# Optimization experiments

Measured on AMD Instinct MI355X. Metric: run time of the kernel, lower is better.

Reference implementation:

```python
import jax, jax.numpy as jnp
import numpy as np

H = 768
NH = 12
HD = H // NH  # 64
WINDOW = 64  # module's self.window_size; band keeps |i-j| <= WINDOW//2


def setup_inputs() -> dict:
    key = jax.random.key(0)
    ks = jax.random.split(key, 9)
    s = 0.02
    return {
        "hidden_states": jax.random.normal(ks[0], (4, 2048, H), dtype=jnp.float32),
        "Wq": jax.random.normal(ks[1], (H, H), dtype=jnp.float32) * s,
        "bq": jnp.zeros((H,), dtype=jnp.float32),
        "Wk": jax.random.normal(ks[2], (H, H), dtype=jnp.float32) * s,
        "bk": jnp.zeros((H,), dtype=jnp.float32),
        "Wv": jax.random.normal(ks[3], (H, H), dtype=jnp.float32) * s,
        "bv": jnp.zeros((H,), dtype=jnp.float32),
        "Wo": jax.random.normal(ks[4], (H, H), dtype=jnp.float32) * s,
        "bo": jnp.zeros((H,), dtype=jnp.float32),
    }


def _attn(hidden_states, Wq, bq, Wk, bk, Wv, bv, Wo, bo):
    B, S, _ = hidden_states.shape
    # projections (torch Linear uses y = x @ W.T + b; here W is stored already transposed)
    q = (hidden_states @ Wq + bq).reshape(B, S, NH, HD).transpose(0, 2, 1, 3)
    k = (hidden_states @ Wk + bk).reshape(B, S, NH, HD).transpose(0, 2, 1, 3)
    v = (hidden_states @ Wv + bv).reshape(B, S, NH, HD).transpose(0, 2, 1, 3)
    # dense scores [B, NH, S, S], faithful to the original O(S^2) computation
    scores = jnp.einsum("bhqd,bhkd->bhqk", q, k) / jnp.sqrt(jnp.float32(HD))
    # sliding-window band mask: keep j in [i - W//2, i + W//2]
    i = jnp.arange(S)[:, None]
    j = jnp.arange(S)[None, :]
    band = jnp.abs(i - j) <= (WINDOW // 2)
    scores = jnp.where(band[None, None, :, :], scores, jnp.float32(-1e9))
    probs = jax.nn.softmax(scores, axis=-1)
    ctx = jnp.einsum("bhqk,bhkd->bhqd", probs, v)
    ctx = ctx.transpose(0, 2, 1, 3).reshape(B, S, H)
    return ctx @ Wo + bo


def reference(hidden_states, Wq, bq, Wk, bk, Wv, bv, Wo, bo):
    return _attn(hidden_states, Wq, bq, Wk, bk, Wv, bv, Wo, bo)
```

## Files before the change

kernel.cpp:

```cpp
#include <hip/hip_runtime.h>
#include <hip/hip_bf16.h>

#define NHEAD 12
#define HD 64
#define SEQ 2048
#define NB 4
#define HDIM 768
#define MTOT (NB * SEQ)

typedef float f32x4 __attribute__((ext_vector_type(4)));
typedef float f32x16 __attribute__((ext_vector_type(16)));
typedef short s16x8 __attribute__((ext_vector_type(8)));
typedef unsigned short u16x8 __attribute__((ext_vector_type(8)));

__device__ inline unsigned short f2bf(float f) {
    union { float f; unsigned u; } v; v.f = f;
    unsigned r = v.u + 0x7fffu + ((v.u >> 16) & 1u);
    return (unsigned short)(r >> 16);
}
__device__ inline float bf2f(unsigned short u) {
    union { unsigned u; float f; } v; v.u = ((unsigned)u) << 16;
    return v.f;
}
__device__ inline unsigned pack_bf2(float a, float b) {
    return (unsigned)f2bf(a) | ((unsigned)f2bf(b) << 16);
}
__device__ inline s16x8 mk_frag(uint2 lo, uint2 hi) {
    union { unsigned u[4]; s16x8 v; } r;
    r.u[0] = lo.x; r.u[1] = lo.y; r.u[2] = hi.x; r.u[3] = hi.y;
    return r.v;
}
__device__ inline void gload_lds16(const unsigned short* g, void* lds_base) {
    __builtin_amdgcn_global_load_lds(
        (const __attribute__((address_space(1))) void*)g,
        (__attribute__((address_space(3))) void*)lds_base, 16, 0, 0);
}

#define MFMA(acc, a, b) \
    acc = __builtin_amdgcn_mfma_f32_16x16x32_bf16((a), (b), (acc), 0, 0, 0)
#define MFMA32(acc, a, b) \
    acc = __builtin_amdgcn_mfma_f32_32x32x16_bf16((a), (b), (acc), 0, 0, 0)

__global__ __launch_bounds__(256) void prep_kernel(
    const float* __restrict__ X,
    const float* __restrict__ Wq, const float* __restrict__ Wk,
    const float* __restrict__ Wv, const float* __restrict__ Wo,
    unsigned short* __restrict__ Xb,
    unsigned short* __restrict__ Wt, unsigned short* __restrict__ Wot)
{
    __shared__ __align__(16) unsigned short ts[64][68];
    const int t = threadIdx.x;
    const int bid = blockIdx.x;

    if (bid < 3072) {
        const int i = (bid * 256 + t) * 8;
        float4 a = *(const float4*)(X + i);
        float4 b = *(const float4*)(X + i + 4);
        ushort4 wa, wb;
        wa.x = f2bf(a.x); wa.y = f2bf(a.y); wa.z = f2bf(a.z); wa.w = f2bf(a.w);
        wb.x = f2bf(b.x); wb.y = f2bf(b.y); wb.z = f2bf(b.z); wb.w = f2bf(b.w);
        *(ushort4*)(Xb + i) = wa;
        *(ushort4*)(Xb + i + 4) = wb;
        return;
    }

    const int id = bid - 3072;
    const int z  = id / 144;
    const int rem = id - z * 144;
    const int k0 = (rem / 12) * 64, n0 = (rem % 12) * 64;
    const float* W = (z == 0) ? Wq : (z == 1) ? Wk : (z == 2) ? Wv : Wo;
    unsigned short* D = (z < 3) ? (Wt + (size_t)z * HDIM * HDIM) : Wot;

    const int kr = (t >> 4) * 4;
    const int nc = (t & 15) * 4;
    #pragma unroll
    for (int r = 0; r < 4; r++) {
        float4 v = *(const float4*)(W + (size_t)(k0 + kr + r) * HDIM + n0 + nc);
        ushort4 w;
        w.x = f2bf(v.x); w.y = f2bf(v.y); w.z = f2bf(v.z); w.w = f2bf(v.w);
        *(ushort4*)&ts[kr + r][nc] = w;
    }
    __syncthreads();
    const int nr = t >> 2;
    const int kc = (t & 3) * 16;
    #pragma unroll
    for (int j4 = 0; j4 < 4; j4++) {
        ushort4 w;
        w.x = ts[kc + j4 * 4 + 0][nr];
        w.y = ts[kc + j4 * 4 + 1][nr];
        w.z = ts[kc + j4 * 4 + 2][nr];
        w.w = ts[kc + j4 * 4 + 3][nr];
        *(ushort4*)(D + (size_t)(n0 + nr) * HDIM + k0 + kc + j4 * 4) = w;
    }
}

template<int MODE, int BM>
__global__ __launch_bounds__(256) void gemm_kernel(
    const unsigned short* __restrict__ A,
    const unsigned short* __restrict__ Bt,
    const float* __restrict__ bias0, const float* __restrict__ bias1,
    const float* __restrict__ bias2,
    unsigned short* __restrict__ Qb, unsigned short* __restrict__ Kb,
    unsigned short* __restrict__ Vb, float* __restrict__ out)
{
    constexpr int MF  = BM / 64;
    constexpr int CHA = BM / 32;

    __shared__ __align__(16) unsigned short As[BM * 64];
    __shared__ __align__(16) unsigned short Bs[128 * 64];

    const int t = threadIdx.x;
    const int lane = t & 63;
    const int wid = t >> 6;
    const int wm = wid >> 1, wn = wid & 1;
    const int l31 = lane & 31;
    const int lh = lane >> 5;

    const int m0 = blockIdx.x * BM;
    const int n0 = blockIdx.y * 128;

    int srow[4], scol[4];
    #pragma unroll
    for (int i = 0; i < 4; i++) {
        const int p = i * 4096 + t * 16;
        const int row = p >> 7;
        const int cb = p & 127;
        srow[i] = row;
        scol[i] = (cb ^ ((row & 7) << 4)) >> 1;
    }

    f32x16 acc[MF][2] = {};

    for (int k0 = 0; k0 < HDIM; k0 += 64) {
        __syncthreads();
        #pragma unroll
        for (int i = 0; i < CHA; i++)
            gload_lds16(A + (size_t)(m0 + srow[i]) * HDIM + k0 + scol[i],
                        (char*)As + i * 4096 + wid * 1024);
        #pragma unroll
        for (int i = 0; i < 4; i++)
            gload_lds16(Bt + (size_t)(n0 + srow[i]) * HDIM + k0 + scol[i],
                        (char*)Bs + i * 4096 + wid * 1024);
        __syncthreads();

        const int sw = (l31 & 7) << 4;
        #pragma unroll
        for (int kv = 0; kv < 4; kv++) {
            const int cb = (kv * 32 + lh * 16) ^ sw;
            s16x8 av[MF];
            #pragma unroll
            for (int j = 0; j < MF; j++)
                av[j] = *(const s16x8*)((const char*)As +
                        (wm * (BM / 2) + j * 32 + l31) * 128 + cb);
            s16x8 b0 = *(const s16x8*)((const char*)Bs + (wn * 64 +      l31) * 128 + cb);
            s16x8 b1 = *(const s16x8*)((const char*)Bs + (wn * 64 + 32 + l31) * 128 + cb);
            #pragma unroll
            for (int j = 0; j < MF; j++) {
                MFMA32(acc[j][0], av[j], b0);
                MFMA32(acc[j][1], av[j], b1);
            }
        }
    }

    if (MODE == 0) {
        const int z = n0 / HDIM;
        const float* bias = (z == 0) ? bias0 : (z == 1) ? bias1 : bias2;
        const float scale = (z == 0) ? 0.125f : 1.0f;
        unsigned short* dst = (z == 0) ? Qb : (z == 1) ? Kb : Vb;
        #pragma unroll
        for (int fm = 0; fm < MF; fm++) {
            #pragma unroll
            for (int fn = 0; fn < 2; fn++) {
                const int coll = (n0 - z * HDIM) + wn * 64 + fn * 32 + l31;
                const float bc = bias[coll];
                const int h = coll >> 6, d = coll & 63;
                #pragma unroll
                for (int reg = 0; reg < 16; reg++) {
                    const int rowD = (reg & 3) + 8 * (reg >> 2) + 4 * lh;
                    const int m = m0 + wm * (BM / 2) + fm * 32 + rowD;
                    const int b = m >> 11, s = m & (SEQ - 1);
                    const size_t idx = (z == 2)
                        ? ((((size_t)b * NHEAD + h) * HD + d) * SEQ + s)
                        : ((((size_t)b * NHEAD + h) * SEQ + s) * HD + d);
                    dst[idx] = f2bf((acc[fm][fn][reg] + bc) * scale);
                }
            }
        }
    } else {
        #pragma unroll
        for (int fm = 0; fm < MF; fm++) {
            #pragma unroll
            for (int fn = 0; fn < 2; fn++) {
                const int col = n0 + wn * 64 + fn * 32 + l31;
                const float bc = bias0[col];
                #pragma unroll
                for (int reg = 0; reg < 16; reg++) {
                    const int rowD = (reg & 3) + 8 * (reg >> 2) + 4 * lh;
                    const int m = m0 + wm * (BM / 2) + fm * 32 + rowD;
                    out[(size_t)m * HDIM + col] = acc[fm][fn][reg] + bc;
                }
            }
        }
    }
}

__global__ __launch_bounds__(512) void attn_mfma(
    const unsigned short* __restrict__ Qb, const unsigned short* __restrict__ Kb,
    const unsigned short* __restrict__ Vtg, unsigned short* __restrict__ Cb)
{
    __shared__ __align__(16) unsigned short Ks[192][72];
    __shared__ __align__(16) unsigned short Vs[64][208];

    const int t = threadIdx.x;
    const int lane = t & 63;
    const int wq = t >> 6;
    const int woff = wq * 16;
    const int g = lane >> 4, r16 = lane & 15;

    const int lid = blockIdx.y * 16 + blockIdx.x;
    const int wg = (lid & 7) * 96 + (lid >> 3);
    const int q0 = (wg & 15) * 128;
    const int bh = wg >> 4;

    const int b = bh / NHEAD, h = bh - b * NHEAD;
    const size_t base  = (size_t)bh * SEQ * HD;
    const size_t vbase = (size_t)bh * HD * SEQ;
    const int kstart = q0 - 32;
    const bool interior = (kstart >= 0) && (kstart + 191 < SEQ);

    #pragma unroll
    for (int i = 0; i < 3; i++) {
        const int u = i * 512 + t;
        const int row = u >> 3, c16 = (u & 7) * 8;
        const int s = kstart + row;
        if (s >= 0 && s < SEQ) {
            *(u16x8*)&Ks[row][c16] =
                *(const u16x8*)(Kb + base + (size_t)s * HD + c16);
        } else {
            const u16x8 z = {};
            *(u16x8*)&Ks[row][c16] = z;
        }
    }
    {
        const int row = t >> 3, c0 = (t & 7) * 24;
        const unsigned short* src = Vtg + vbase + (size_t)row * SEQ + kstart + c0;
        if (interior) {
            #pragma unroll
            for (int j = 0; j < 3; j++)
                *(u16x8*)&Vs[row][c0 + 8 * j] = *(const u16x8*)(src + 8 * j);
        } else {
            for (int e = 0; e < 24; e++) {
                const int s = kstart + c0 + e;
                Vs[row][c0 + e] = (s >= 0 && s < SEQ) ? src[e] : (unsigned short)0;
            }
        }
        if (t < 128) {
            const u16x8 z = {};
            *(u16x8*)&Vs[t >> 1][192 + (t & 1) * 8] = z;
        }
    }

    s16x8 qf[2];
    {
        const unsigned short* gq = Qb + base + (size_t)(q0 + woff + r16) * HD;
        #pragma unroll
        for (int c = 0; c < 2; c++)
            qf[c] = mk_frag(*(const uint2*)(gq + c * 32 + 4 * g),
                            *(const uint2*)(gq + c * 32 + 16 + 4 * g));
    }
    __syncthreads();

    f32x4 sacc[5] = {};
    #pragma unroll
    for (int mf = 0; mf < 5; mf++) {
        const unsigned short* p = &Ks[woff + mf * 16 + r16][0];
        #pragma unroll
        for (int c = 0; c < 2; c++) {
            s16x8 kf = mk_frag(*(const uint2*)(p + c * 32 + 4 * g),
                               *(const uint2*)(p + c * 32 + 16 + 4 * g));
            MFMA(sacc[mf], kf, qf[c]);
        }
    }

    float mx = -1e30f;
    #pragma unroll
    for (int mf = 0; mf < 5; mf++) {
        #pragma unroll
        for (int r = 0; r < 4; r++) {
            const int rel = mf * 16 + 4 * g + r - r16;
            const int sg = kstart + woff + mf * 16 + 4 * g + r;
            const bool ok = (rel >= 0) && (rel <= 64) && (sg >= 0) && (sg < SEQ);
            const float v = ok ? sacc[mf][r] : -1e30f;
            sacc[mf][r] = v;
            mx = fmaxf(mx, v);
        }
    }
    mx = fmaxf(mx, __shfl_xor(mx, 16));
    mx = fmaxf(mx, __shfl_xor(mx, 32));
    float l = 0.f;
    #pragma unroll
    for (int mf = 0; mf < 5; mf++) {
        #pragma unroll
        for (int r = 0; r < 4; r++) {
            const float e = __expf(sacc[mf][r] - mx);
            sacc[mf][r] = e;
            l += e;
        }
    }
    l += __shfl_xor(l, 16);
    l += __shfl_xor(l, 32);
    const float inv = 1.f / l;

    s16x8 pf[3];
    #pragma unroll
    for (int c = 0; c < 3; c++) {
        union { unsigned u[4]; s16x8 v; } pv;
        pv.u[0] = pack_bf2(sacc[2 * c][0] * inv, sacc[2 * c][1] * inv);
        pv.u[1] = pack_bf2(sacc[2 * c][2] * inv, sacc[2 * c][3] * inv);
        if (c < 2) {
            pv.u[2] = pack_bf2(sacc[2 * c + 1][0] * inv, sacc[2 * c + 1][1] * inv);
            pv.u[3] = pack_bf2(sacc[2 * c + 1][2] * inv, sacc[2 * c + 1][3] * inv);
        } else {
            pv.u[2] = 0; pv.u[3] = 0;
        }
        pf[c] = pv.v;
    }

    f32x4 cacc[4] = {};
    #pragma unroll
    for (int nf = 0; nf < 4; nf++) {
        const unsigned short* p = &Vs[nf * 16 + r16][woff];
        #pragma unroll
        for (int c = 0; c < 3; c++) {
            s16x8 vf = mk_frag(*(const uint2*)(p + c * 32 + 4 * g),
                               *(const uint2*)(p + c * 32 + 16 + 4 * g));
            MFMA(cacc[nf], pf[c], vf);
        }
    }

    #pragma unroll
    for (int nf = 0; nf < 4; nf++) {
        #pragma unroll
        for (int r = 0; r < 4; r++) {
            const int ql = woff + 4 * g + r;
            const int d = nf * 16 + r16;
            Cb[(((size_t)b * SEQ + q0 + ql) * NHEAD + h) * HD + d] = f2bf(cacc[nf][r]);
        }
    }
}

extern "C" void kernel_launch(void* const* d_in, const int* in_sizes, int n_in,
                              void* d_out, int out_size, void* d_ws, size_t ws_size,
                              hipStream_t stream)
{
    const float* X  = (const float*)d_in[0];
    const float* Wq = (const float*)d_in[1];
    const float* bq = (const float*)d_in[2];
    const float* Wk = (const float*)d_in[3];
    const float* bk = (const float*)d_in[4];
    const float* Wv = (const float*)d_in[5];
    const float* bv = (const float*)d_in[6];
    const float* Wo = (const float*)d_in[7];
    const float* bo = (const float*)d_in[8];
    float* out = (float*)d_out;

    char* ws = (char*)d_ws;
    unsigned short* Xb  = (unsigned short*)ws;
    unsigned short* Cb  = Xb;
    unsigned short* Vt  = (unsigned short*)(ws + 12582912);
    unsigned short* Wtp = (unsigned short*)(ws + 25165824);
    unsigned short* Wot = (unsigned short*)(ws + 28704768);
    unsigned short* Qb  = (unsigned short*)d_out;
    unsigned short* Kb  = (unsigned short*)((char*)d_out + 12582912);

    prep_kernel<<<dim3(3648), 256, 0, stream>>>(X, Wq, Wk, Wv, Wo, Xb, Wtp, Wot);
    gemm_kernel<0, 64><<<dim3(128, 18), 256, 0, stream>>>(Xb, Wtp, bq, bk, bv, Qb, Kb, Vt, nullptr);
    attn_mfma<<<dim3(16, 48), 512, 0, stream>>>(Qb, Kb, Vt, Cb);
    gemm_kernel<1, 64><<<dim3(128, 6), 256, 0, stream>>>(Cb, Wot, bo, nullptr, nullptr,
                                                         nullptr, nullptr, nullptr, out);
}
```

Measured before the change: 107.7 us.

## Fuse X fp32-to-bf16 conversion into QKV GEMM and coalesce attention output stores

Removes the separate X conversion pass from the prep kernel. The QKV GEMM now loads fp32 X directly, converts it to bf16 in registers and writes it into swizzled LDS, with the M tile raised to 128. The attention epilogue stages its context tile through LDS so global stores are 16-byte vectors instead of scattered 2-byte writes. This saves a full bf16 round trip of X through memory and improves store coalescing, at the cost of synchronous register-staged A loads instead of direct global-to-LDS, plus extra barriers in attention.

```diff
diff --git a/kernel.cpp b/kernel.cpp
--- a/kernel.cpp
+++ b/kernel.cpp
@@ -42,29 +42,13 @@
     acc = __builtin_amdgcn_mfma_f32_32x32x16_bf16((a), (b), (acc), 0, 0, 0)
 
 __global__ __launch_bounds__(256) void prep_kernel(
-    const float* __restrict__ X,
     const float* __restrict__ Wq, const float* __restrict__ Wk,
     const float* __restrict__ Wv, const float* __restrict__ Wo,
-    unsigned short* __restrict__ Xb,
     unsigned short* __restrict__ Wt, unsigned short* __restrict__ Wot)
 {
     __shared__ __align__(16) unsigned short ts[64][68];
     const int t = threadIdx.x;
-    const int bid = blockIdx.x;
-
-    if (bid < 3072) {
-        const int i = (bid * 256 + t) * 8;
-        float4 a = *(const float4*)(X + i);
-        float4 b = *(const float4*)(X + i + 4);
-        ushort4 wa, wb;
-        wa.x = f2bf(a.x); wa.y = f2bf(a.y); wa.z = f2bf(a.z); wa.w = f2bf(a.w);
-        wb.x = f2bf(b.x); wb.y = f2bf(b.y); wb.z = f2bf(b.z); wb.w = f2bf(b.w);
-        *(ushort4*)(Xb + i) = wa;
-        *(ushort4*)(Xb + i + 4) = wb;
-        return;
-    }
-
-    const int id = bid - 3072;
+    const int id = blockIdx.x;
     const int z  = id / 144;
     const int rem = id - z * 144;
     const int k0 = (rem / 12) * 64, n0 = (rem % 12) * 64;
@@ -96,6 +80,7 @@
 
 template<int MODE, int BM>
 __global__ __launch_bounds__(256) void gemm_kernel(
+    const float* __restrict__ Xf,
     const unsigned short* __restrict__ A,
     const unsigned short* __restrict__ Bt,
     const float* __restrict__ bias0, const float* __restrict__ bias1,
@@ -119,27 +104,49 @@
     const int m0 = blockIdx.x * BM;
     const int n0 = blockIdx.y * 128;
 
-    int srow[4], scol[4];
+    int srow[4], scb[4], sswb[4];
     #pragma unroll
     for (int i = 0; i < 4; i++) {
         const int p = i * 4096 + t * 16;
         const int row = p >> 7;
         const int cb = p & 127;
         srow[i] = row;
-        scol[i] = (cb ^ ((row & 7) << 4)) >> 1;
+        scb[i] = cb;
+        sswb[i] = cb ^ ((row & 7) << 4);
     }
 
     f32x16 acc[MF][2] = {};
 
     for (int k0 = 0; k0 < HDIM; k0 += 64) {
+        float4 fa[CHA][2];
+        if (MODE == 0) {
+            #pragma unroll
+            for (int i = 0; i < CHA; i++) {
+                const float* src = Xf + (size_t)(m0 + srow[i]) * HDIM + k0 + (scb[i] >> 1);
+                fa[i][0] = *(const float4*)src;
+                fa[i][1] = *(const float4*)(src + 4);
+            }
+        }
         __syncthreads();
-        #pragma unroll
-        for (int i = 0; i < CHA; i++)
-            gload_lds16(A + (size_t)(m0 + srow[i]) * HDIM + k0 + scol[i],
-                        (char*)As + i * 4096 + wid * 1024);
+        if (MODE == 0) {
+            #pragma unroll
+            for (int i = 0; i < CHA; i++) {
+                u16x8 w;
+                w[0] = f2bf(fa[i][0].x); w[1] = f2bf(fa[i][0].y);
+                w[2] = f2bf(fa[i][0].z); w[3] = f2bf(fa[i][0].w);
+                w[4] = f2bf(fa[i][1].x); w[5] = f2bf(fa[i][1].y);
+                w[6] = f2bf(fa[i][1].z); w[7] = f2bf(fa[i][1].w);
+                *(u16x8*)((char*)As + srow[i] * 128 + sswb[i]) = w;
+            }
+        } else {
+            #pragma unroll
+            for (int i = 0; i < CHA; i++)
+                gload_lds16(A + (size_t)(m0 + srow[i]) * HDIM + k0 + (sswb[i] >> 1),
+                            (char*)As + i * 4096 + wid * 1024);
+        }
         #pragma unroll
         for (int i = 0; i < 4; i++)
-            gload_lds16(Bt + (size_t)(n0 + srow[i]) * HDIM + k0 + scol[i],
+            gload_lds16(Bt + (size_t)(n0 + srow[i]) * HDIM + k0 + (sswb[i] >> 1),
                         (char*)Bs + i * 4096 + wid * 1024);
         __syncthreads();
 
@@ -338,14 +345,25 @@
         }
     }
 
+    __syncthreads();
+    unsigned short* Cs = &Ks[0][0];
     #pragma unroll
     for (int nf = 0; nf < 4; nf++) {
         #pragma unroll
         for (int r = 0; r < 4; r++) {
             const int ql = woff + 4 * g + r;
             const int d = nf * 16 + r16;
-            Cb[(((size_t)b * SEQ + q0 + ql) * NHEAD + h) * HD + d] = f2bf(cacc[nf][r]);
-        }
+            Cs[ql * 72 + d] = f2bf(cacc[nf][r]);
+        }
+    }
+    __syncthreads();
+
+    #pragma unroll
+    for (int i = 0; i < 2; i++) {
+        const int u = i * 512 + t;
+        const int row = u >> 3, c16 = (u & 7) * 8;
+        u16x8 w = *(const u16x8*)&Cs[row * 72 + c16];
+        *(u16x8*)(Cb + (((size_t)b * SEQ + q0 + row) * NHEAD + h) * HD + c16) = w;
     }
 }
 
@@ -365,17 +383,17 @@
     float* out = (float*)d_out;
 
     char* ws = (char*)d_ws;
-    unsigned short* Xb  = (unsigned short*)ws;
-    unsigned short* Cb  = Xb;
+    unsigned short* Cb  = (unsigned short*)ws;
     unsigned short* Vt  = (unsigned short*)(ws + 12582912);
     unsigned short* Wtp = (unsigned short*)(ws + 25165824);
     unsigned short* Wot = (unsigned short*)(ws + 28704768);
     unsigned short* Qb  = (unsigned short*)d_out;
     unsigned short* Kb  = (unsigned short*)((char*)d_out + 12582912);
 
-    prep_kernel<<<dim3(3648), 256, 0, stream>>>(X, Wq, Wk, Wv, Wo, Xb, Wtp, Wot);
-    gemm_kernel<0, 64><<<dim3(128, 18), 256, 0, stream>>>(Xb, Wtp, bq, bk, bv, Qb, Kb, Vt, nullptr);
+    prep_kernel<<<dim3(576), 256, 0, stream>>>(Wq, Wk, Wv, Wo, Wtp, Wot);
+    gemm_kernel<0, 128><<<dim3(64, 18), 256, 0, stream>>>(X, nullptr, Wtp, bq, bk, bv,
+                                                          Qb, Kb, Vt, nullptr);
     attn_mfma<<<dim3(16, 48), 512, 0, stream>>>(Qb, Kb, Vt, Cb);
-    gemm_kernel<1, 64><<<dim3(128, 6), 256, 0, stream>>>(Cb, Wot, bo, nullptr, nullptr,
-                                                         nullptr, nullptr, nullptr, out);
-}
+    gemm_kernel<1, 64><<<dim3(128, 6), 256, 0, stream>>>(nullptr, Cb, Wot, bo, nullptr,
+                                                         nullptr, nullptr, nullptr, nullptr, out);
+}
```

Result: slower. 114.9 us (+6.7%).
